# Performance work log

Measured on AMD Instinct MI355X. Metric: run time of the kernel, lower is better.

The kernel has to match this reference:

```python
import jax, jax.numpy as jnp
import numpy as np

N_EMBD = 768
N_HEAD = 12
HEAD_DIM = N_EMBD // N_HEAD  # 64


def setup_inputs() -> dict:
    key = jax.random.key(0)
    k1, k2, k3 = jax.random.split(key, 3)
    B, S = 4, 2048
    x = jax.random.normal(k1, (B, S, N_EMBD), dtype=jnp.float32)
    W_attn = jax.random.normal(k2, (N_EMBD, 3 * N_EMBD), dtype=jnp.float32) * 0.02
    b_attn = jax.random.normal(k3, (3 * N_EMBD,), dtype=jnp.float32) * 0.02
    return {"x": x, "W_attn": W_attn, "b_attn": b_attn}


def reference(x, W_attn, b_attn):
    B, S, E = x.shape
    H, D = N_HEAD, HEAD_DIM
    # fused QKV projection (torch Linear: x @ W^T + b; here W_attn stored as [E, 3E])
    qkv = x @ W_attn + b_attn  # [B, S, 3E]
    q, k, v = jnp.split(qkv, 3, axis=-1)
    q = q.reshape(B, S, H, D)
    k = k.reshape(B, S, H, D)
    v = v.reshape(B, S, H, D)
    scale = 1.0 / np.sqrt(D).astype(np.float32)
    scores = jnp.einsum('bqhd,bkhd->bhqk', q, k) * scale  # [B, H, S, S]
    causal = jnp.tril(jnp.ones((S, S), dtype=bool))
    # ReLU attention nonlinearity (no softmax); masked entries -> 0
    att = jnp.where(causal, jnp.maximum(scores, 0.0), 0.0)
    y = jnp.einsum('bhqk,bkhd->bqhd', att, v)  # [B, S, H, D]
    return y.reshape(B, S, E)
```

## Files before the change

### kernel.cpp

```cpp
#include <hip/hip_runtime.h>

typedef __attribute__((ext_vector_type(8))) short short8;
typedef __attribute__((ext_vector_type(4))) short short4v;
typedef __attribute__((ext_vector_type(4))) float floatx4;
typedef __attribute__((ext_vector_type(2))) unsigned int uint2v;

#define S_LEN 2048
#define NH 12
#define HD 64
#define EMB 768
#define E3 2304

__device__ __forceinline__ unsigned short f2bf(float f) {
    unsigned int u = __builtin_bit_cast(unsigned int, f);
    u += 0x7FFFu + ((u >> 16) & 1u);
    return (unsigned short)(u >> 16);
}

__device__ __forceinline__ unsigned int pack2bf(float a, float b) {
#if __has_builtin(__builtin_amdgcn_cvt_pk_bf16_f32)
    typedef __attribute__((ext_vector_type(2))) short short2v;
    short2v r = __builtin_amdgcn_cvt_pk_bf16_f32(a, b);
    return __builtin_bit_cast(unsigned int, r);
#else
    return (unsigned int)f2bf(a) | ((unsigned int)f2bf(b) << 16);
#endif
}

__device__ __forceinline__ void gl_lds16(const void* g, void* l) {
    __builtin_amdgcn_global_load_lds(
        (const __attribute__((address_space(1))) unsigned int*)g,
        (__attribute__((address_space(3))) unsigned int*)l, 16, 0, 0);
}

__global__ __launch_bounds__(256) void conv_fused(const float* __restrict__ x,
                                                  ushort* __restrict__ xb,
                                                  const float* __restrict__ W,
                                                  ushort* __restrict__ Wt) {
    int tid = threadIdx.x;
    if (blockIdx.x < 6144) {
        int i = (blockIdx.x * 256 + tid) * 4;
        float4 f = *(const float4*)(x + i);
        ushort4 o;
        o.x = f2bf(f.x); o.y = f2bf(f.y); o.z = f2bf(f.z); o.w = f2bf(f.w);
        *(ushort4*)(xb + i) = o;
    } else {
        __shared__ float tile[32][33];
        int b2 = blockIdx.x - 6144;
        int n0 = (b2 % 72) * 32, k0 = (b2 / 72) * 32;
        int tx = tid & 31, ty = tid >> 5;
        for (int i = 0; i < 4; i++)
            tile[ty + i * 8][tx] = W[(size_t)(k0 + ty + i * 8) * E3 + n0 + tx];
        __syncthreads();
        for (int i = 0; i < 4; i++)
            Wt[(size_t)(n0 + ty + i * 8) * EMB + k0 + tx] = f2bf(tile[tx][ty + i * 8]);
    }
}

__global__ __launch_bounds__(256) void qkv_gemm(const ushort* __restrict__ Xb,
                                                const ushort* __restrict__ Wt,
                                                const float* __restrict__ bias,
                                                ushort* __restrict__ QKb,
                                                ushort* __restrict__ Vt) {
    __shared__ ushort lds[16896];
    char* ldsb = (char*)lds;
    int tid  = threadIdx.x;
    int wv = tid >> 6, lane = tid & 63;
    int l15 = lane & 15, quad = lane >> 4;
    int r8 = lane >> 3, cc = lane & 7;
    int wm = wv >> 1, wn = wv & 1;
    int m0 = blockIdx.x * 128, n0 = blockIdx.y * 128;

    floatx4 acc[4][4] = {};

    const char* ag = (const char*)(Xb + (size_t)m0 * EMB)
                   + (wv * 32 + r8) * 1536 + (cc ^ r8) * 16;
    const char* bgp = (const char*)(Wt + (size_t)n0 * EMB)
                   + (wv * 32 + r8) * 1536 + (cc ^ r8) * 16;
    int ast = (wv * 32) * 128;
    int bst = 16384 + (wv * 32) * 128;
    int afo[2], bfo[2];
    for (int ch = 0; ch < 2; ch++) {
        int sw = ((ch * 4 + quad) ^ (l15 & 7)) * 16;
        afo[ch] = wm * 8192 + l15 * 128 + sw;
        bfo[ch] = 16384 + wn * 8192 + l15 * 128 + sw;
    }

    for (int k0 = 0; k0 < 12; k0++) {
        __syncthreads();
        for (int i = 0; i < 4; i++) {
            gl_lds16(ag + i * 12288, ldsb + ast + i * 1024);
            gl_lds16(bgp + i * 12288, ldsb + bst + i * 1024);
        }
        ag += 128;  bgp += 128;
        __syncthreads();
        for (int ch = 0; ch < 2; ch++) {
            short8 af[4], bf[4];
            for (int mi = 0; mi < 4; mi++)
                af[mi] = *(const short8*)(ldsb + afo[ch] + mi * 2048);
            for (int ni = 0; ni < 4; ni++)
                bf[ni] = *(const short8*)(ldsb + bfo[ch] + ni * 2048);
            for (int mi = 0; mi < 4; mi++)
                for (int ni = 0; ni < 4; ni++)
                    acc[mi][ni] = __builtin_amdgcn_mfma_f32_16x16x32_bf16(
                        af[mi], bf[ni], acc[mi][ni], 0, 0, 0);
        }
    }

    __syncthreads();
    int seg = n0 / EMB;
    if (seg < 2) {
        float scale = (seg == 0) ? 0.125f : 1.0f;
        for (int ni = 0; ni < 4; ni++) {
            int nl = wn * 64 + ni * 16 + l15;
            float bv = bias[n0 + nl];
            for (int mi = 0; mi < 4; mi++)
                for (int r = 0; r < 4; r++) {
                    int ml = wm * 64 + mi * 16 + quad * 4 + r;
                    lds[ml * 132 + nl] = f2bf((acc[mi][ni][r] + bv) * scale);
                }
        }
        __syncthreads();
        int row = tid >> 1, half2 = tid & 1;
        size_t gm = (size_t)(m0 + row);
        for (int i = 0; i < 8; i++) {
            uint4 v = *(const uint4*)&lds[row * 132 + half2 * 64 + i * 8];
            *(uint4*)&QKb[gm * 1536 + n0 + half2 * 64 + i * 8] = v;
        }
    } else {
        for (int ni = 0; ni < 4; ni++) {
            int nl = wn * 64 + ni * 16 + l15;
            float bv = bias[n0 + nl];
            for (int mi = 0; mi < 4; mi++) {
                int ml = wm * 64 + mi * 16 + quad * 4;
                ushort4 p4;
                p4.x = f2bf(acc[mi][ni][0] + bv);
                p4.y = f2bf(acc[mi][ni][1] + bv);
                p4.z = f2bf(acc[mi][ni][2] + bv);
                p4.w = f2bf(acc[mi][ni][3] + bv);
                *(ushort4*)&lds[nl * 132 + ml] = p4;
            }
        }
        __syncthreads();
        int row = tid >> 1, half2 = tid & 1;
        int nn = n0 + row - 1536;
        int hh = nn >> 6, d = nn & 63;
        int bb = m0 >> 11, s0 = m0 & 2047;
        for (int i = 0; i < 8; i++) {
            uint4 v = *(const uint4*)&lds[row * 132 + half2 * 64 + i * 8];
            *(uint4*)&Vt[((size_t)(bb * NH + hh) * HD + d) * S_LEN + s0 + half2 * 64 + i * 8] = v;
        }
    }
}

__global__ __launch_bounds__(128) void attn(const ushort* __restrict__ QKb,
                                            const ushort* __restrict__ Vt,
                                            float* __restrict__ out) {
    __shared__ ushort lds[32768];
    char* ldsb = (char*)lds;
    int tid = threadIdx.x;
    int w = tid >> 6, lane = tid & 63;
    int l15 = lane & 15, quad = lane >> 4;
    int r8 = lane >> 3, cc = lane & 7;
    int qh = quad >> 1, qlo = quad & 1;

    int g = blockIdx.x / 48, bh = blockIdx.x % 48;
    int qt = w ? (15 - g) : (31 - g);
    int bg = bh / NH, h = bh % NH;

    const char* Kb = (const char*)(QKb + (size_t)bg * S_LEN * 1536 + 768 + h * 64)
                   + r8 * 3072 + (cc ^ r8) * 16;
    const char* Vb = (const char*)(Vt + (size_t)bh * HD * S_LEN)
                   + r8 * 4096 + (cc ^ r8) * 16;
    const ushort* Qcol = QKb + (size_t)bg * S_LEN * 1536 + h * 64;

    int wb = w * 32768;
    int kfo[2];
    for (int ch = 0; ch < 2; ch++)
        kfo[ch] = wb + l15 * 128 + (((ch * 4 + quad) ^ (l15 & 7)) * 16);
    int vfo[4];
    for (int kb = 0; kb < 4; kb++)
        vfo[kb] = wb + 8192 + l15 * 128 + (((kb * 2 + qh) ^ (l15 & 7)) * 16) + qlo * 8;

    for (int i = 0; i < 8; i++)
        gl_lds16(Kb + i * 24576, ldsb + wb + i * 1024);
    for (int i = 0; i < 8; i++)
        gl_lds16(Vb + i * 32768, ldsb + wb + 8192 + i * 1024);

    short8 qf[4][2];
    for (int nq = 0; nq < 4; nq++)
        for (int ch = 0; ch < 2; ch++)
            qf[nq][ch] = *(const short8*)(Qcol +
                (size_t)(qt * 64 + nq * 16 + l15) * 1536 + ch * 32 + quad * 8);

    floatx4 acco[4][4] = {};
    int p = 0;
    for (int st = 0; st <= qt; st++) {
        if (st < qt) {
            const char* ks = Kb + (size_t)(st + 1) * 196608;
            const char* vs = Vb + (st + 1) * 128;
            int d = wb + (p ^ 1) * 16384;
            for (int i = 0; i < 8; i++)
                gl_lds16(ks + i * 24576, ldsb + d + i * 1024);
            for (int i = 0; i < 8; i++)
                gl_lds16(vs + i * 32768, ldsb + d + 8192 + i * 1024);
            asm volatile("s_waitcnt vmcnt(16)" ::: "memory");
        } else {
            asm volatile("s_waitcnt vmcnt(0)" ::: "memory");
        }
        int pb = p * 16384;
        bool diag = (st == qt);

        short4v vf[4][4];
        for (int kb = 0; kb < 4; kb++)
            for (int ni = 0; ni < 4; ni++)
                vf[kb][ni] = *(const short4v*)(ldsb + pb + vfo[kb] + ni * 2048);
        short8 kf[4][2];
        for (int mk = 0; mk < 4; mk++)
            for (int ch = 0; ch < 2; ch++)
                kf[mk][ch] = *(const short8*)(ldsb + pb + kfo[ch] + mk * 2048);

        for (int nq = 0; nq < 4; nq++) {
            floatx4 stc[4] = {};
            for (int ch = 0; ch < 2; ch++)
                for (int mk = 0; mk < 4; mk++)
                    stc[mk] = __builtin_amdgcn_mfma_f32_16x16x32_bf16(
                        kf[mk][ch], qf[nq][ch], stc[mk], 0, 0, 0);
            unsigned int pk[4][2];
            for (int mk = 0; mk < 4; mk++) {
                float e[4];
                for (int r = 0; r < 4; r++) e[r] = fmaxf(stc[mk][r], 0.0f);
                if (diag) {
                    int kl = mk * 16 + quad * 4;
                    int ql = nq * 16 + l15;
                    for (int r = 0; r < 4; r++)
                        if (kl + r > ql) e[r] = 0.0f;
                }
                pk[mk][0] = pack2bf(e[0], e[1]);
                pk[mk][1] = pack2bf(e[2], e[3]);
            }
            for (int mk = 0; mk < 4; mk++) {
                short4v a = __builtin_bit_cast(short4v, (uint2v){pk[mk][0], pk[mk][1]});
                for (int ni = 0; ni < 4; ni++)
                    acco[nq][ni] = __builtin_amdgcn_mfma_f32_16x16x16bf16_1k(
                        a, vf[mk][ni], acco[nq][ni], 0, 0, 0);
            }
        }
        p ^= 1;
    }

    for (int nq = 0; nq < 4; nq++) {
        for (int ni = 0; ni < 4; ni++) {
            int d = ni * 16 + l15;
            for (int r = 0; r < 4; r++) {
                int s = qt * 64 + nq * 16 + quad * 4 + r;
                out[((size_t)bg * S_LEN + s) * EMB + h * 64 + d] = acco[nq][ni][r];
            }
        }
    }
}

extern "C" void kernel_launch(void* const* d_in, const int* in_sizes, int n_in,
                              void* d_out, int out_size, void* d_ws, size_t ws_size,
                              hipStream_t stream) {
    const float* x    = (const float*)d_in[0];
    const float* W    = (const float*)d_in[1];
    const float* bias = (const float*)d_in[2];
    float* out = (float*)d_out;

    char* ws = (char*)d_ws;
    const size_t SZ_X  = (size_t)8192 * EMB * 2;
    const size_t SZ_W  = (size_t)E3 * EMB * 2;
    const size_t SZ_QK = (size_t)8192 * 1536 * 2;
    ushort* Xb  = (ushort*)(ws);
    ushort* Wt  = (ushort*)(ws + SZ_X);
    ushort* QKb = (ushort*)(ws + SZ_X + SZ_W);
    ushort* Vt  = (ushort*)(ws + SZ_X + SZ_W + SZ_QK);

    conv_fused<<<dim3(6144 + 1728), dim3(256), 0, stream>>>(x, Xb, W, Wt);
    qkv_gemm<<<dim3(64, 18), dim3(256), 0, stream>>>(Xb, Wt, bias, QKb, Vt);
    attn<<<dim3(768), dim3(128), 0, stream>>>(QKb, Vt, out);
}
```

Measured before the change: 202.1 us.

## Rebalance causal attention work with three waves per block and half-size key tiles

The attention kernel now launches 512 blocks of three independent waves instead of 768 blocks of two. Each wave takes one (query tile, head) item from a triple-pairing scheme over the 1536 items, so per-block causal work is more even. Key/value stages shrink from 64 to 32 keys, with a new V swizzle and a diagonal mask that tracks the key offset, cutting LDS per wave and making the double-buffered stages finer. In exchange there are more loop iterations and barriers per wave, and fewer MFMAs per stage to hide load latency.

```diff
diff --git a/kernel.cpp b/kernel.cpp
--- a/kernel.cpp
+++ b/kernel.cpp
@@ -153,39 +153,44 @@
     }
 }
 
-__global__ __launch_bounds__(128) void attn(const ushort* __restrict__ QKb,
+__global__ __launch_bounds__(192) void attn(const ushort* __restrict__ QKb,
                                             const ushort* __restrict__ Vt,
                                             float* __restrict__ out) {
-    __shared__ ushort lds[32768];
+    __shared__ ushort lds[24576];
     char* ldsb = (char*)lds;
     int tid = threadIdx.x;
     int w = tid >> 6, lane = tid & 63;
     int l15 = lane & 15, quad = lane >> 4;
     int r8 = lane >> 3, cc = lane & 7;
-    int qh = quad >> 1, qlo = quad & 1;
-
-    int g = blockIdx.x / 48, bh = blockIdx.x % 48;
-    int qt = w ? (15 - g) : (31 - g);
+    int rv = lane >> 2, c4 = lane & 3;
+
+    int b = blockIdx.x;
+    int g = (w == 0) ? b : (w == 1 ? 512 + b : 1535 - b);
+    int qt = 31 - g / 48;
+    int bh = g % 48;
     int bg = bh / NH, h = bh % NH;
 
     const char* Kb = (const char*)(QKb + (size_t)bg * S_LEN * 1536 + 768 + h * 64)
                    + r8 * 3072 + (cc ^ r8) * 16;
     const char* Vb = (const char*)(Vt + (size_t)bh * HD * S_LEN)
-                   + r8 * 4096 + (cc ^ r8) * 16;
+                   + rv * 4096 + ((c4 ^ (rv & 3)) * 16);
     const ushort* Qcol = QKb + (size_t)bg * S_LEN * 1536 + h * 64;
 
-    int wb = w * 32768;
-    int kfo[2];
-    for (int ch = 0; ch < 2; ch++)
-        kfo[ch] = wb + l15 * 128 + (((ch * 4 + quad) ^ (l15 & 7)) * 16);
-    int vfo[4];
-    for (int kb = 0; kb < 4; kb++)
-        vfo[kb] = wb + 8192 + l15 * 128 + (((kb * 2 + qh) ^ (l15 & 7)) * 16) + qlo * 8;
-
-    for (int i = 0; i < 8; i++)
+    int wb = w * 16384;
+    int kfo[2][2];
+    for (int mk = 0; mk < 2; mk++)
+        for (int ch = 0; ch < 2; ch++)
+            kfo[mk][ch] = wb + (mk * 16 + l15) * 128 + (((ch * 4 + quad) ^ (l15 & 7)) * 16);
+    int vfo[2][4];
+    for (int mk = 0; mk < 2; mk++)
+        for (int ni = 0; ni < 4; ni++)
+            vfo[mk][ni] = wb + 4096 + (ni * 16 + l15) * 64
+                        + (((2 * mk + (quad >> 1)) ^ (l15 & 3)) * 16) + (quad & 1) * 8;
+
+    for (int i = 0; i < 4; i++)
         gl_lds16(Kb + i * 24576, ldsb + wb + i * 1024);
-    for (int i = 0; i < 8; i++)
-        gl_lds16(Vb + i * 32768, ldsb + wb + 8192 + i * 1024);
+    for (int i = 0; i < 4; i++)
+        gl_lds16(Vb + (size_t)i * 65536, ldsb + wb + 4096 + i * 1024);
 
     short8 qf[4][2];
     for (int nq = 0; nq < 4; nq++)
@@ -194,53 +199,51 @@
                 (size_t)(qt * 64 + nq * 16 + l15) * 1536 + ch * 32 + quad * 8);
 
     floatx4 acco[4][4] = {};
+    int nst = 2 * qt + 2;
     int p = 0;
-    for (int st = 0; st <= qt; st++) {
-        if (st < qt) {
-            const char* ks = Kb + (size_t)(st + 1) * 196608;
-            const char* vs = Vb + (st + 1) * 128;
-            int d = wb + (p ^ 1) * 16384;
-            for (int i = 0; i < 8; i++)
+    for (int st = 0; st < nst; st++) {
+        if (st + 1 < nst) {
+            const char* ks = Kb + (size_t)(st + 1) * 98304;
+            const char* vs = Vb + (st + 1) * 64;
+            int d = wb + (p ^ 1) * 8192;
+            for (int i = 0; i < 4; i++)
                 gl_lds16(ks + i * 24576, ldsb + d + i * 1024);
-            for (int i = 0; i < 8; i++)
-                gl_lds16(vs + i * 32768, ldsb + d + 8192 + i * 1024);
-            asm volatile("s_waitcnt vmcnt(16)" ::: "memory");
+            for (int i = 0; i < 4; i++)
+                gl_lds16(vs + (size_t)i * 65536, ldsb + d + 4096 + i * 1024);
+            asm volatile("s_waitcnt vmcnt(8)" ::: "memory");
         } else {
             asm volatile("s_waitcnt vmcnt(0)" ::: "memory");
         }
-        int pb = p * 16384;
-        bool diag = (st == qt);
-
-        short4v vf[4][4];
-        for (int kb = 0; kb < 4; kb++)
+        int pb = p * 8192;
+        int base = 32 * st - 64 * qt;
+        bool diag = (base >= 0);
+
+        short8 kf[2][2];
+        for (int mk = 0; mk < 2; mk++)
+            for (int ch = 0; ch < 2; ch++)
+                kf[mk][ch] = *(const short8*)(ldsb + pb + kfo[mk][ch]);
+        short4v vf[2][4];
+        for (int mk = 0; mk < 2; mk++)
             for (int ni = 0; ni < 4; ni++)
-                vf[kb][ni] = *(const short4v*)(ldsb + pb + vfo[kb] + ni * 2048);
-        short8 kf[4][2];
-        for (int mk = 0; mk < 4; mk++)
+                vf[mk][ni] = *(const short4v*)(ldsb + pb + vfo[mk][ni]);
+
+        for (int nq = 0; nq < 4; nq++) {
+            floatx4 stc[2] = {};
             for (int ch = 0; ch < 2; ch++)
-                kf[mk][ch] = *(const short8*)(ldsb + pb + kfo[ch] + mk * 2048);
-
-        for (int nq = 0; nq < 4; nq++) {
-            floatx4 stc[4] = {};
-            for (int ch = 0; ch < 2; ch++)
-                for (int mk = 0; mk < 4; mk++)
+                for (int mk = 0; mk < 2; mk++)
                     stc[mk] = __builtin_amdgcn_mfma_f32_16x16x32_bf16(
                         kf[mk][ch], qf[nq][ch], stc[mk], 0, 0, 0);
-            unsigned int pk[4][2];
-            for (int mk = 0; mk < 4; mk++) {
+            for (int mk = 0; mk < 2; mk++) {
                 float e[4];
                 for (int r = 0; r < 4; r++) e[r] = fmaxf(stc[mk][r], 0.0f);
                 if (diag) {
-                    int kl = mk * 16 + quad * 4;
+                    int kl = base + mk * 16 + quad * 4;
                     int ql = nq * 16 + l15;
                     for (int r = 0; r < 4; r++)
                         if (kl + r > ql) e[r] = 0.0f;
                 }
-                pk[mk][0] = pack2bf(e[0], e[1]);
-                pk[mk][1] = pack2bf(e[2], e[3]);
-            }
-            for (int mk = 0; mk < 4; mk++) {
-                short4v a = __builtin_bit_cast(short4v, (uint2v){pk[mk][0], pk[mk][1]});
+                short4v a = __builtin_bit_cast(short4v,
+                             (uint2v){pack2bf(e[0], e[1]), pack2bf(e[2], e[3])});
                 for (int ni = 0; ni < 4; ni++)
                     acco[nq][ni] = __builtin_amdgcn_mfma_f32_16x16x16bf16_1k(
                         a, vf[mk][ni], acco[nq][ni], 0, 0, 0);
@@ -279,5 +282,5 @@
 
     conv_fused<<<dim3(6144 + 1728), dim3(256), 0, stream>>>(x, Xb, W, Wt);
     qkv_gemm<<<dim3(64, 18), dim3(256), 0, stream>>>(Xb, Wt, bias, QKb, Vt);
-    attn<<<dim3(768), dim3(128), 0, stream>>>(QKb, Vt, out);
-}
+    attn<<<dim3(512), dim3(192), 0, stream>>>(QKb, Vt, out);
+}
```

Result: slower. 220.6 us (+9.1%).
